# Kernel optimization log

Hardware: AMD Instinct MI355X
Metric: run time of the kernel (lower is better)

## Reference

```python
import jax, jax.numpy as jnp
import numpy as np

B, S, R = 8192, 256, 8192  # gas cells, species, reactions


def setup_inputs() -> dict:
    key = jax.random.key(0)
    ks = jax.random.split(key, 10)
    abundances = jax.random.uniform(ks[0], (B, S), jnp.float32, 1e-12, 1.0)
    temperature = jax.random.uniform(ks[1], (B,), jnp.float32, 10.0, 300.0)
    cr_rate = jax.random.uniform(ks[2], (B,), jnp.float32, 0.1, 10.0)
    fuv_rate = jax.random.uniform(ks[3], (B,), jnp.float32, 0.1, 10.0)
    time = jnp.zeros((B,), jnp.float32)  # unused by the RHS, kept for signature parity
    incidence = jax.random.normal(ks[4], (S, R), jnp.float32)  # stoichiometry matrix
    alpha = jax.random.uniform(ks[5], (R,), jnp.float32, 1e-12, 1e-9)
    beta = jax.random.normal(ks[6], (R,), jnp.float32) * 0.5
    gamma = jax.random.uniform(ks[7], (R,), jnp.float32, 0.0, 100.0)
    # species index or S (== out-of-bounds sentinel -> fill_value 1.0, i.e. <2 reactants)
    reactant_multipliers = jax.random.randint(ks[8], (R, 2), 0, S + 1, jnp.int32)
    rtype = jax.random.randint(ks[9], (R,), 0, 3, jnp.int32)  # 0: Arrhenius, 1: CR, 2: FUV
    return {
        'time': time, 'abundances': abundances, 'temperature': temperature,
        'cr_rate': cr_rate, 'fuv_rate': fuv_rate, 'incidence': incidence,
        'alpha': alpha, 'beta': beta, 'gamma': gamma,
        'reactant_multipliers': reactant_multipliers, 'rtype': rtype,
    }


def _get_rates(temperature, cr_rate, fuv_rate, alpha, beta, gamma, rtype):
    # JNetwork.get_rates: hstack of per-reaction rate terms -> (B, R)
    T = temperature[:, None]                                      # (B, 1)
    k_arr = alpha * jnp.exp(beta * jnp.log(T / 300.0) - gamma / T)  # Arrhenius
    k_cr = alpha * cr_rate[:, None]                               # cosmic-ray driven
    k_fuv = alpha * jnp.exp(-gamma) * fuv_rate[:, None]           # FUV photorate
    return jnp.where(rtype == 0, k_arr, jnp.where(rtype == 1, k_cr, k_fuv))


def reference(time, abundances, temperature, cr_rate, fuv_rate,
              incidence, alpha, beta, gamma, reactant_multipliers, rtype):
    rates = _get_rates(temperature, cr_rate, fuv_rate, alpha, beta, gamma, rtype)
    # multiply_rates_by_abundance: gather reactant abundances (mode='drop',
    # fill_value=1.0) and reduce with a product over the 2 reactant slots.
    ones_col = jnp.ones((abundances.shape[0], 1), abundances.dtype)
    ab_pad = jnp.concatenate([abundances, ones_col], axis=1)      # (B, S+1), col S == 1.0
    prod = ab_pad[:, reactant_multipliers[:, 0]] * ab_pad[:, reactant_multipliers[:, 1]]  # (B, R)
    flux = rates * prod                                           # (B, R)
    # incidence @ rates, batched: (S, R) x (B, R) -> (B, S)
    return jnp.einsum('sr,br->bs', incidence, flux)
```

## Files before the change

kernel.cpp:

```cpp
#include <hip/hip_runtime.h>
#include <stdint.h>

typedef __bf16 bf16;
typedef __bf16 bf16x8 __attribute__((ext_vector_type(8)));
typedef float  f32x4  __attribute__((ext_vector_type(4)));

#if __has_builtin(__builtin_amdgcn_exp2f)
#define EXP2F(x) __builtin_amdgcn_exp2f(x)
#else
#define EXP2F(x) exp2f(x)
#endif

#define GLD_LDS16(g, l)                                                                    \
  __builtin_amdgcn_global_load_lds((const __attribute__((address_space(1))) uint32_t*)(g), \
                                   (__attribute__((address_space(3))) uint32_t*)(l), 16, 0, 0)

constexpr int Bn = 8192, Sn = 256, Rn = 8192;
constexpr int BM = 64, BK = 32, KP = 4;
constexpr int KLEN = Rn / KP;
constexpr int NC = KLEN / BK;

__global__ __launch_bounds__(256) void build_perm(const int* __restrict__ rtype,
                                                  int* __restrict__ perm) {
  __shared__ int c0[256], c1[256], c2[256];
  const int t = threadIdx.x;
  const int base = t * 32;
  int4 vv[8];
  const int4* rp = (const int4*)(rtype + base);
#pragma unroll
  for (int k = 0; k < 8; ++k) vv[k] = rp[k];
  int ty[32];
#pragma unroll
  for (int k = 0; k < 8; ++k) {
    ty[k * 4 + 0] = vv[k].x; ty[k * 4 + 1] = vv[k].y;
    ty[k * 4 + 2] = vv[k].z; ty[k * 4 + 3] = vv[k].w;
  }
  int l0 = 0, l1 = 0, l2 = 0;
#pragma unroll
  for (int i = 0; i < 32; ++i) {
    int v = ty[i];
    l0 += (v == 0); l1 += (v == 1); l2 += (v == 2);
  }
  c0[t] = l0; c1[t] = l1; c2[t] = l2;
  __syncthreads();
  for (int off = 1; off < 256; off <<= 1) {
    int a = (t >= off) ? c0[t - off] : 0;
    int b = (t >= off) ? c1[t - off] : 0;
    int c = (t >= off) ? c2[t - off] : 0;
    __syncthreads();
    c0[t] += a; c1[t] += b; c2[t] += c;
    __syncthreads();
  }
  const int tot0 = c0[255], tot1 = c1[255];
  int o0 = c0[t] - l0;
  int o1 = tot0 + c1[t] - l1;
  int o2 = tot0 + tot1 + c2[t] - l2;
#pragma unroll
  for (int i = 0; i < 32; ++i) {
    int v = ty[i];
    int pos = (v == 0) ? o0++ : ((v == 1) ? o1++ : o2++);
    perm[pos] = base + i;
  }
}

__global__ __launch_bounds__(256) void prep_all(
    const float* __restrict__ inc, bf16* __restrict__ incb,
    const float* __restrict__ alpha, const float* __restrict__ beta,
    const float* __restrict__ gam, const int* __restrict__ rm, const int* __restrict__ rtype,
    float4* __restrict__ params, const float* __restrict__ temp,
    const float* __restrict__ cr, const float* __restrict__ fuv, float4* __restrict__ perb,
    const int* __restrict__ perm) {
  const int g = blockIdx.x, tid = threadIdx.x;
  size_t e = ((size_t)g * 256 + tid) * 8;
  int n = (int)(e >> 13);
  int kpos = (int)(e & 8191);
  int sw = (n >> 1) & 3;
  int src = (kpos & ~31) | (((((kpos >> 3) & 3)) ^ sw) << 3);
  const int* pp = perm + src;
  const float* rowp = inc + ((size_t)n << 13);
  bf16x8 o;
#pragma unroll
  for (int i = 0; i < 8; ++i) o[i] = (bf16)rowp[pp[i]];
  *(bf16x8*)(incb + e) = o;
  if (g < 32) {
    int p = g * 256 + tid;
    int r = perm[p];
    float a = alpha[r], be = beta[r], gm = gam[r];
    int ty = rtype[r];
    int i0 = rm[2 * r], i1 = rm[2 * r + 1];
    float x, P = 0.0f, Q = 0.0f;
    if (ty == 0) { x = __log2f(a); P = be; Q = gm; }
    else if (ty == 1) { x = a; }
    else { x = a * expf(-gm); }
    uint32_t bits = (uint32_t)i0 | ((uint32_t)i1 << 10) | ((uint32_t)ty << 20);
    params[p] = make_float4(x, P, Q, __uint_as_float(bits));
  } else if (g < 64) {
    int b = (g - 32) * 256 + tid;
    float T = temp[b];
    perb[b] = make_float4(__log2f(T * (1.0f / 300.0f)), 1.4426950408889634f / T,
                          cr[b], fuv[b]);
  }
}

__global__ __launch_bounds__(256, 2) void flux_gemm(
    const float* __restrict__ abund, const float4* __restrict__ perb,
    const float4* __restrict__ params, const bf16* __restrict__ incb,
    float* __restrict__ partial) {
  __shared__ bf16 ab_lds[257 * 64];
  __shared__ bf16 inc_lds[2][256 * BK];
  __shared__ bf16 flux_lds[2][64 * BK];

  const int tid  = threadIdx.x;
  const int lane = tid & 63;
  const int w    = tid >> 6;
  const int ws   = __builtin_amdgcn_readfirstlane(w);
  const int x   = blockIdx.x & 7;
  const int jb  = blockIdx.x >> 3;
  const int kp  = x & 3;
  const int m0g = (jb * 2 + (x >> 2)) * BM;
  const int kstart = kp * KLEN;
  const int r16 = lane & 15, q = lane >> 4;
  const int sw16 = (r16 >> 1) & 3;
  const int fsw  = w ^ ((lane >> 1) & 3);

#pragma unroll
  for (int i = 0; i < 4; ++i) {
    int rrow = w * 64 + i * 16 + (lane >> 2);
    const bf16* gp = incb + (size_t)rrow * Rn + kstart + (lane & 3) * 8;
    GLD_LDS16(gp, inc_lds[0] + (w * 64 + i * 16) * BK);
  }

  {
    int bsub = tid >> 2;
    int scol = (tid & 3) * 64;
    const float* rowp = abund + (size_t)(m0g + bsub) * Sn + scol;
#pragma unroll
    for (int j = 0; j < 16; ++j) {
      float4 v = *(const float4*)(rowp + j * 4);
      int s = scol + j * 4;
      ab_lds[(s + 0) * 64 + bsub] = (bf16)v.x;
      ab_lds[(s + 1) * 64 + bsub] = (bf16)v.y;
      ab_lds[(s + 2) * 64 + bsub] = (bf16)v.z;
      ab_lds[(s + 3) * 64 + bsub] = (bf16)v.w;
    }
    if (tid < 64) ab_lds[256 * 64 + tid] = (bf16)1.0f;
  }

  float4 pb = perb[m0g + lane];
  const float l2t = pb.x, nitv = -pb.y, crv = pb.z, fuvv = pb.w;

  auto flux_tile = [&](int kb, int buf) {
    const float4* pw = params + kb + ws * 8;
    float4 pr[8];
#pragma unroll
    for (int j = 0; j < 8; ++j) pr[j] = pw[j];
    uint32_t b0 = __builtin_amdgcn_readfirstlane(__float_as_uint(pr[0].w));
    uint32_t b7 = __builtin_amdgcn_readfirstlane(__float_as_uint(pr[7].w));
    uint32_t t0 = b0 >> 20, t7 = b7 >> 20;
    bf16x8 fv;
    if (t0 == 0 && t7 == 0) {
#pragma unroll
      for (int j = 0; j < 8; ++j) {
        uint32_t bits = __builtin_amdgcn_readfirstlane(__float_as_uint(pr[j].w));
        int i0 = (int)(bits & 1023), i1 = (int)((bits >> 10) & 1023);
        float a0 = (float)ab_lds[i0 * 64 + lane];
        float a1 = (float)ab_lds[i1 * 64 + lane];
        float v = EXP2F(fmaf(pr[j].y, l2t, fmaf(pr[j].z, nitv, pr[j].x)));
        fv[j] = (bf16)(v * (a0 * a1));
      }
    } else if (t0 == t7) {
      float mv = (t0 == 1) ? crv : fuvv;
#pragma unroll
      for (int j = 0; j < 8; ++j) {
        uint32_t bits = __builtin_amdgcn_readfirstlane(__float_as_uint(pr[j].w));
        int i0 = (int)(bits & 1023), i1 = (int)((bits >> 10) & 1023);
        float a0 = (float)ab_lds[i0 * 64 + lane];
        float a1 = (float)ab_lds[i1 * 64 + lane];
        fv[j] = (bf16)((pr[j].x * mv) * (a0 * a1));
      }
    } else {
#pragma unroll
      for (int j = 0; j < 8; ++j) {
        uint32_t bits = __builtin_amdgcn_readfirstlane(__float_as_uint(pr[j].w));
        int i0 = (int)(bits & 1023), i1 = (int)((bits >> 10) & 1023), ms = (int)(bits >> 20);
        float a0 = (float)ab_lds[i0 * 64 + lane];
        float a1 = (float)ab_lds[i1 * 64 + lane];
        float ve = EXP2F(fmaf(pr[j].y, l2t, fmaf(pr[j].z, nitv, pr[j].x)));
        float vm = pr[j].x * ((ms == 1) ? crv : fuvv);
        float v = (ms == 0) ? ve : vm;
        fv[j] = (bf16)(v * (a0 * a1));
      }
    }
    *(bf16x8*)(flux_lds[buf] + lane * BK + fsw * 8) = fv;
  };

  __syncthreads();

  flux_tile(kstart, 0);

  f32x4 acc[4][4];
#pragma unroll
  for (int i = 0; i < 4; ++i)
#pragma unroll
    for (int j = 0; j < 4; ++j) acc[i][j] = (f32x4)0.0f;

  for (int c = 0; c < NC; ++c) {
    const int cur = c & 1, nxt = cur ^ 1;
    __syncthreads();

    bf16x8 af[4], bfr[4];
#pragma unroll
    for (int mt = 0; mt < 4; ++mt)
      af[mt] = *(const bf16x8*)(flux_lds[cur] + (mt * 16 + r16) * BK + (q ^ sw16) * 8);
#pragma unroll
    for (int nt = 0; nt < 4; ++nt)
      bfr[nt] = *(const bf16x8*)(inc_lds[cur] + (w * 64 + nt * 16 + r16) * BK + (q ^ sw16) * 8);

    if (c + 1 < NC) {
      const int kb = kstart + (c + 1) * BK;
#pragma unroll
      for (int i = 0; i < 4; ++i) {
        int rrow = w * 64 + i * 16 + (lane >> 2);
        const bf16* gp = incb + (size_t)rrow * Rn + kb + (lane & 3) * 8;
        GLD_LDS16(gp, inc_lds[nxt] + (w * 64 + i * 16) * BK);
      }
      flux_tile(kb, nxt);
    }

    __builtin_amdgcn_s_setprio(1);
#pragma unroll
    for (int mt = 0; mt < 4; ++mt)
#pragma unroll
      for (int nt = 0; nt < 4; ++nt)
        acc[mt][nt] = __builtin_amdgcn_mfma_f32_16x16x32_bf16(af[mt], bfr[nt], acc[mt][nt], 0, 0, 0);
    __builtin_amdgcn_s_setprio(0);
  }

  float* pout = partial + (size_t)kp * Bn * Sn;
#pragma unroll
  for (int mt = 0; mt < 4; ++mt)
#pragma unroll
    for (int nt = 0; nt < 4; ++nt) {
      int col = w * 64 + nt * 16 + r16;
      int row = m0g + mt * 16 + q * 4;
#pragma unroll
      for (int rg = 0; rg < 4; ++rg)
        pout[(size_t)(row + rg) * Sn + col] = acc[mt][nt][rg];
    }
}

__global__ __launch_bounds__(256) void reduce_k(const float* __restrict__ partial,
                                               float* __restrict__ out) {
  size_t i = ((size_t)blockIdx.x * 256 + threadIdx.x) * 4;
  constexpr size_t NS = (size_t)Bn * Sn;
  float4 a = *(const float4*)(partial + i);
  float4 b = *(const float4*)(partial + NS + i);
  float4 c = *(const float4*)(partial + 2 * NS + i);
  float4 d = *(const float4*)(partial + 3 * NS + i);
  float4 r;
  r.x = (a.x + b.x) + (c.x + d.x);
  r.y = (a.y + b.y) + (c.y + d.y);
  r.z = (a.z + b.z) + (c.z + d.z);
  r.w = (a.w + b.w) + (c.w + d.w);
  *(float4*)(out + i) = r;
}

extern "C" void kernel_launch(void* const* d_in, const int* in_sizes, int n_in,
                              void* d_out, int out_size, void* d_ws, size_t ws_size,
                              hipStream_t stream) {
  const float* abund = (const float*)d_in[1];
  const float* temp  = (const float*)d_in[2];
  const float* cr    = (const float*)d_in[3];
  const float* fuv   = (const float*)d_in[4];
  const float* inc   = (const float*)d_in[5];
  const float* alpha = (const float*)d_in[6];
  const float* beta  = (const float*)d_in[7];
  const float* gam   = (const float*)d_in[8];
  const int*   rm    = (const int*)d_in[9];
  const int*   rty   = (const int*)d_in[10];
  float* out = (float*)d_out;

  float4* params  = (float4*)d_ws;
  float4* perb    = params + Rn;
  bf16*   incb    = (bf16*)(perb + Bn);
  float*  partial = (float*)(incb + (size_t)Sn * Rn);
  int*    perm    = (int*)partial;

  build_perm<<<1, 256, 0, stream>>>(rty, perm);
  prep_all<<<1024, 256, 0, stream>>>(inc, incb, alpha, beta, gam, rm, rty,
                                     params, temp, cr, fuv, perb, perm);
  flux_gemm<<<(Bn / BM) * KP, 256, 0, stream>>>(abund, perb, params, incb, partial);
  reduce_k<<<(Bn * Sn) / 1024, 256, 0, stream>>>(partial, out);
}
```

Baseline: 166.6 us.

## Load incidence fragments directly from global in tiled layout, drop LDS staging

The prep kernel now writes the bf16 incidence matrix in a chunk-tiled layout ([kp][chunk][row][32]), so each wave's MFMA B fragments are contiguous 16-byte pieces. The GEMM reads these fragments straight from global/L2 into registers instead of staging them through double-buffered LDS with global_load_lds. This frees LDS, which could raise occupancy, and removes the LDS traffic. In exchange the global loads are issued in the same iteration they are consumed, so their latency is not prefetched ahead and the MFMAs may stall.

```diff
diff --git a/kernel.cpp b/kernel.cpp
--- a/kernel.cpp
+++ b/kernel.cpp
@@ -10,10 +10,6 @@
 #else
 #define EXP2F(x) exp2f(x)
 #endif
-
-#define GLD_LDS16(g, l)                                                                    \
-  __builtin_amdgcn_global_load_lds((const __attribute__((address_space(1))) uint32_t*)(g), \
-                                   (__attribute__((address_space(3))) uint32_t*)(l), 16, 0, 0)
 
 constexpr int Bn = 8192, Sn = 256, Rn = 8192;
 constexpr int BM = 64, BK = 32, KP = 4;
@@ -72,12 +68,12 @@
     const int* __restrict__ perm) {
   const int g = blockIdx.x, tid = threadIdx.x;
   size_t e = ((size_t)g * 256 + tid) * 8;
-  int n = (int)(e >> 13);
-  int kpos = (int)(e & 8191);
-  int sw = (n >> 1) & 3;
-  int src = (kpos & ~31) | (((((kpos >> 3) & 3)) ^ sw) << 3);
-  const int* pp = perm + src;
-  const float* rowp = inc + ((size_t)n << 13);
+  int col8 = (int)(e & 31);
+  int row  = (int)((e >> 5) & 255);
+  int c    = (int)((e >> 13) & 63);
+  int kp   = (int)(e >> 19);
+  const int* pp = perm + (kp * KLEN + c * BK + col8);
+  const float* rowp = inc + ((size_t)row << 13);
   bf16x8 o;
 #pragma unroll
   for (int i = 0; i < 8; ++i) o[i] = (bf16)rowp[pp[i]];
@@ -107,7 +103,6 @@
     const float4* __restrict__ params, const bf16* __restrict__ incb,
     float* __restrict__ partial) {
   __shared__ bf16 ab_lds[257 * 64];
-  __shared__ bf16 inc_lds[2][256 * BK];
   __shared__ bf16 flux_lds[2][64 * BK];
 
   const int tid  = threadIdx.x;
@@ -122,13 +117,6 @@
   const int r16 = lane & 15, q = lane >> 4;
   const int sw16 = (r16 >> 1) & 3;
   const int fsw  = w ^ ((lane >> 1) & 3);
-
-#pragma unroll
-  for (int i = 0; i < 4; ++i) {
-    int rrow = w * 64 + i * 16 + (lane >> 2);
-    const bf16* gp = incb + (size_t)rrow * Rn + kstart + (lane & 3) * 8;
-    GLD_LDS16(gp, inc_lds[0] + (w * 64 + i * 16) * BK);
-  }
 
   {
     int bsub = tid >> 2;
@@ -204,28 +192,24 @@
 #pragma unroll
     for (int j = 0; j < 4; ++j) acc[i][j] = (f32x4)0.0f;
 
+  const bf16* bbase = incb + (size_t)(kp * NC) * 8192 + (w * 64 + r16) * BK + q * 8;
+
   for (int c = 0; c < NC; ++c) {
     const int cur = c & 1, nxt = cur ^ 1;
     __syncthreads();
 
-    bf16x8 af[4], bfr[4];
+    bf16x8 bfr[4];
+    const bf16* bp = bbase + (size_t)c * 8192;
+#pragma unroll
+    for (int nt = 0; nt < 4; ++nt)
+      bfr[nt] = *(const bf16x8*)(bp + nt * (16 * BK));
+
+    bf16x8 af[4];
 #pragma unroll
     for (int mt = 0; mt < 4; ++mt)
       af[mt] = *(const bf16x8*)(flux_lds[cur] + (mt * 16 + r16) * BK + (q ^ sw16) * 8);
-#pragma unroll
-    for (int nt = 0; nt < 4; ++nt)
-      bfr[nt] = *(const bf16x8*)(inc_lds[cur] + (w * 64 + nt * 16 + r16) * BK + (q ^ sw16) * 8);
-
-    if (c + 1 < NC) {
-      const int kb = kstart + (c + 1) * BK;
-#pragma unroll
-      for (int i = 0; i < 4; ++i) {
-        int rrow = w * 64 + i * 16 + (lane >> 2);
-        const bf16* gp = incb + (size_t)rrow * Rn + kb + (lane & 3) * 8;
-        GLD_LDS16(gp, inc_lds[nxt] + (w * 64 + i * 16) * BK);
-      }
-      flux_tile(kb, nxt);
-    }
+
+    if (c + 1 < NC) flux_tile(kstart + (c + 1) * BK, nxt);
 
     __builtin_amdgcn_s_setprio(1);
 #pragma unroll
```

After: 159.5 us. 1.04x faster.
